# Performance work log

Hardware: AMD Instinct MI355X
Metric: run time of the kernel (lower is better)

Reference implementation:

```python
import jax, jax.numpy as jnp
import numpy as np

B, L, D = 16, 1024, 512
MAX_LEN = 1024  # module hardcodes self.max_len = 1024


def setup_inputs() -> dict:
    key = jax.random.key(0)
    k0, k1, k2, k3, k4 = jax.random.split(key, 5)
    s = 1.0 / np.sqrt(D)
    return {
        "x": jax.random.normal(k0, (B, L, D), jnp.float32),
        "generator": 0.02 * jax.random.normal(k1, (D, 2 * MAX_LEN - 1), jnp.float32),
        "Wq": jax.random.normal(k2, (D, D), jnp.float32) * s,
        "Wv": jax.random.normal(k3, (D, D), jnp.float32) * s,
        "Wc": jax.random.normal(k4, (D, D), jnp.float32) * s,
    }


def reference(x, generator, Wq, Wv, Wc):
    Bc, Lc, Dc = x.shape
    q = x @ Wq.T                      # (B, L, D)
    v = x @ Wv.T                      # (B, L, D)
    # extract_center_window: window of size 2L-1 centered at MAX_LEN-1
    center_full = (generator.shape[-1] + 1) // 2  # == MAX_LEN
    gen = generator[:, center_full - Lc: center_full + Lc - 1]  # (D, 2L-1)
    w = jnp.einsum('bld,di->bli', q, gen)  # (B, L, 2L-1)
    # Toeplitz gather: out[b, l, i] = w[b, l, (L-1) - l + i]
    r = jnp.arange(Lc)
    idx = (Lc - 1) - r[:, None] + r[None, :]  # (L, L)
    w = jnp.take_along_axis(w, idx[None, :, :], axis=-1)  # (B, L, L)
    w = jnp.cumsum(w, axis=1)
    w = jax.nn.relu(w)
    w = jnp.tril(w)
    w = w / (jnp.sum(w, axis=-1, keepdims=True) + 1e-8)
    out = jnp.einsum('bli,bid->bld', w, v)  # (B, L, D)
    return out @ Wc.T
```

## Files before the change

kernel.cpp:

```cpp
#include <hip/hip_runtime.h>
#include <hip/hip_bf16.h>

typedef __attribute__((ext_vector_type(8))) __bf16 bf16x8;
typedef __attribute__((ext_vector_type(4))) __bf16 bf16x4;
typedef __attribute__((ext_vector_type(4))) float  f32x4;

__device__ __forceinline__ void gl_lds16(const __bf16* g, __bf16* l) {
  __builtin_amdgcn_global_load_lds(
      (const __attribute__((address_space(1))) void*)g,
      (__attribute__((address_space(3))) void*)l,
      16, 0, 0);
}


__global__ __launch_bounds__(256) void prep_kernel(
    const float* __restrict__ x, const float* __restrict__ gen,
    const float* __restrict__ Wq, const float* __restrict__ Wv, const float* __restrict__ Wc,
    __bf16* __restrict__ xb, __bf16* __restrict__ genT,
    __bf16* __restrict__ wqT, __bf16* __restrict__ wvT, __bf16* __restrict__ wcb,
    float* __restrict__ gp) {
  __shared__ float S[64][65];
  const int blk = blockIdx.x, tid = threadIdx.x;

  if (blk < 128) {
    const float* in = (blk < 64) ? Wq : Wv;
    __bf16* out = (blk < 64) ? wqT : wvT;
    int t = blk & 63;
    int tx = tid & 63, ty = tid >> 6;
    int d0 = (t >> 3) * 64, e0 = (t & 7) * 64;
#pragma unroll
    for (int i = 0; i < 16; ++i) {
      int di = i * 4 + ty;
      S[di][tx] = in[(long)(d0 + di) * 512 + e0 + tx];
    }
    __syncthreads();
#pragma unroll
    for (int i = 0; i < 16; ++i) {
      int ei = i * 4 + ty;
      out[(long)(e0 + ei) * 512 + d0 + tx] = (__bf16)S[tx][ei];
    }
  } else if (blk < 384) {
    int i = (blk - 128) * 256 + tid;
    float4 v = ((const float4*)Wc)[i];
    bf16x4 o;
    o[0] = (__bf16)v.x; o[1] = (__bf16)v.y; o[2] = (__bf16)v.z; o[3] = (__bf16)v.w;
    *(bf16x4*)(wcb + 4L * i) = o;
  } else if (blk < 2432) {
    int i = blk - 384;
    for (int d = tid; d < 512; d += 256) {
      float v = (i < 2047) ? gen[(long)d * 2047 + i] : 0.f;
      genT[(long)i * 512 + d] = (__bf16)v;
    }
  } else if (blk < 10624) {
    int i = (blk - 2432) * 256 + tid;
    float4 v = ((const float4*)x)[i];
    bf16x4 o;
    o[0] = (__bf16)v.x; o[1] = (__bf16)v.y; o[2] = (__bf16)v.z; o[3] = (__bf16)v.w;
    *(bf16x4*)(xb + 4L * i) = o;
  } else {
    int t = blk - 10624;
    int i = t % 63, c = t / 63;
    int d0 = c * 64, k = tid;
    float a0 = 0.f, a1 = 0.f;
#pragma unroll 8
    for (int u = 0; u < 64; ++u) {
      int d = d0 + u;
      float g = gen[(long)d * 2047 + 992 + i];
      a0 += Wq[(long)d * 512 + k] * g;
      a1 += Wq[(long)d * 512 + k + 256] * g;
    }
    long o = ((long)c * 63 + i) * 512;
    gp[o + k] = a0;
    gp[o + k + 256] = a1;
  }
}

__global__ void g2t_reduce(const float* __restrict__ gp, float* __restrict__ g2t) {
  int idx = blockIdx.x * 256 + threadIdx.x;
  if (idx >= 63 * 512) return;
  float s = 0.f;
#pragma unroll
  for (int c = 0; c < 8; ++c) s += gp[(long)c * 63 * 512 + idx];
  g2t[idx] = s;
}

__device__ __forceinline__ void gemm128_body(
    const __bf16* __restrict__ Ab, const __bf16* __restrict__ Bb,
    __bf16 (*As)[128 * 32], __bf16 (*Bs)[128 * 32],
    int m0, int n0, int K, int nt, f32x4 (&acc)[4][4]) {
  const int tid = threadIdx.x;
  const int w = tid >> 6, l = tid & 63;
  const int srow = w * 16 + (l >> 2);
  const int scol = (((l & 3) ^ ((l >> 3) & 3))) * 8;
  const int wr = (w >> 1) * 64, wc = (w & 1) * 64;
  const int fr = l & 15;
  const int cp = (((l >> 4) ^ ((fr >> 1) & 3))) << 3;

  auto STAGE = [&](int t, int p) {
    const int k0 = t << 5;
    gl_lds16(Ab + (long)(m0 + srow) * K + (k0 + scol),      &As[p][(w * 16) * 32]);
    gl_lds16(Ab + (long)(m0 + 64 + srow) * K + (k0 + scol), &As[p][(64 + w * 16) * 32]);
    gl_lds16(Bb + (long)(n0 + srow) * K + (k0 + scol),      &Bs[p][(w * 16) * 32]);
    gl_lds16(Bb + (long)(n0 + 64 + srow) * K + (k0 + scol), &Bs[p][(64 + w * 16) * 32]);
  };
  STAGE(0, 0);
  if (nt > 1) STAGE(1, 1);
  if (nt > 2) STAGE(2, 2);
  int p = 0;
  for (int t = 0; t < nt; ++t) {
    const int ahead = nt - 1 - t;
    if (ahead >= 2)      asm volatile("s_waitcnt vmcnt(8)\ns_barrier" ::: "memory");
    else if (ahead == 1) asm volatile("s_waitcnt vmcnt(4)\ns_barrier" ::: "memory");
    else                 asm volatile("s_waitcnt vmcnt(0)\ns_barrier" ::: "memory");
    bf16x8 af[4], bg[4];
#pragma unroll
    for (int i = 0; i < 4; ++i) af[i] = *(const bf16x8*)&As[p][(wr + i * 16 + fr) * 32 + cp];
#pragma unroll
    for (int j = 0; j < 4; ++j) bg[j] = *(const bf16x8*)&Bs[p][(wc + j * 16 + fr) * 32 + cp];
    asm volatile("s_waitcnt lgkmcnt(0)\ns_barrier" ::: "memory");
    if (t + 3 < nt) STAGE(t + 3, p);
#pragma unroll
    for (int i = 0; i < 4; ++i)
#pragma unroll
      for (int j = 0; j < 4; ++j)
        acc[i][j] = __builtin_amdgcn_mfma_f32_16x16x32_bf16(af[i], bg[j], acc[i][j], 0, 0, 0);
    p = (p == 2) ? 0 : p + 1;
  }
}

__global__ __launch_bounds__(256) void gemm_fold(
    const __bf16* __restrict__ A1, const __bf16* __restrict__ B1, __bf16* __restrict__ C1,
    const __bf16* __restrict__ A2, const __bf16* __restrict__ B2, __bf16* __restrict__ C2) {
  __shared__ __bf16 As[3][128 * 32];
  __shared__ __bf16 Bs[3][128 * 32];
  const int b = blockIdx.x;
  const __bf16 *Ab, *Bb; __bf16* C; int m0, n0;
  if (b < 16) { Ab = A1; Bb = B1; C = C1; m0 = (b >> 2) * 128; n0 = (b & 3) * 128; }
  else { int t = b - 16; Ab = A2; Bb = B2; C = C2; m0 = (t >> 2) * 128; n0 = (t & 3) * 128; }

  f32x4 acc[4][4] = {};
  gemm128_body(Ab, Bb, As, Bs, m0, n0, 512, 16, acc);

  const int l = threadIdx.x & 63, w = threadIdx.x >> 6;
  const int rbase = m0 + (w >> 1) * 64 + ((l >> 4) << 2);
  const int cbase = n0 + (w & 1) * 64 + (l & 15);
#pragma unroll
  for (int i = 0; i < 4; ++i)
#pragma unroll
    for (int r = 0; r < 4; ++r) {
      long row = rbase + i * 16 + r;
#pragma unroll
      for (int j = 0; j < 4; ++j) C[row * 512 + cbase + j * 16] = (__bf16)acc[i][j][r];
    }
}

__global__ __launch_bounds__(256) void gemm_out(
    const __bf16* __restrict__ A, const __bf16* __restrict__ B, float* __restrict__ Cv,
    const float* __restrict__ aux) {
  __shared__ __bf16 As[3][128 * 32];
  __shared__ __bf16 Bs[3][128 * 32];
  const int m0 = blockIdx.y * 128, n0 = blockIdx.x * 128, bz = blockIdx.z;
  const int K = 1024;
  const __bf16* Ab = A + (long)bz * 1024 * 1024;
  const __bf16* Bb = B + (long)bz * 512 * 1024;
  const int nt = (m0 + 128) >> 5;

  f32x4 acc[4][4] = {};
  gemm128_body(Ab, Bb, As, Bs, m0, n0, K, nt, acc);

  const int l = threadIdx.x & 63, w = threadIdx.x >> 6;
  const int rbase = m0 + (w >> 1) * 64 + ((l >> 4) << 2);
  const int cbase = n0 + (w & 1) * 64 + (l & 15);
  float* C = Cv + (long)bz * 512 * 1024;
  const float* ax = aux + bz * 1024;
#pragma unroll
  for (int i = 0; i < 4; ++i)
#pragma unroll
    for (int r = 0; r < 4; ++r) {
      long row = rbase + i * 16 + r;
      float sc = 1.f / (ax[row] + 1e-8f);
#pragma unroll
      for (int j = 0; j < 4; ++j) C[row * 512 + cbase + j * 16] = acc[i][j][r] * sc;
    }
}

__global__ __launch_bounds__(512) void gemm_x(
    const __bf16* __restrict__ A, const __bf16* __restrict__ Bg,
    const __bf16* __restrict__ Pm, __bf16* __restrict__ S, __bf16* __restrict__ vT) {
  __shared__ __bf16 As[3][256 * 32];
  __shared__ __bf16 Bs[3][128 * 32];
  const int tid = threadIdx.x;
  const int w = tid >> 6, l = tid & 63;

  int wgid = blockIdx.x;
  int swz = (wgid & 7) * 112 + (wgid >> 3);
  int y = swz / 14, xt = swz - y * 14;
  const bool band = (xt < 10);
  const int m0 = y * 256;
  const int n0 = band ? (6 - 2 * (y & 3) + xt) * 128 : (xt - 10) * 128;
  const __bf16* Bb = band ? Bg : Pm;
  const int K = 512;

  const int srow = w * 16 + (l >> 2);
  const int scol = (((l & 3) ^ ((l >> 3) & 3))) * 8;
  const int wr = (w >> 1) * 64;
  const int wc = (w & 1) * 64;
  const int fr = l & 15;
  const int cp = (((l >> 4) ^ ((fr >> 1) & 3))) << 3;

  f32x4 acc[4][4] = {};

  auto STAGE = [&](int t, int p) {
    const int k0 = t << 5;
    gl_lds16(A + (long)(m0 + srow) * K + (k0 + scol),        &As[p][(w * 16) * 32]);
    gl_lds16(A + (long)(m0 + 128 + srow) * K + (k0 + scol),  &As[p][(128 + w * 16) * 32]);
    gl_lds16(Bb + (long)(n0 + srow) * K + (k0 + scol),       &Bs[p][(w * 16) * 32]);
  };

  STAGE(0, 0);
  STAGE(1, 1);
  STAGE(2, 2);

  int p = 0;
  for (int t = 0; t < 16; ++t) {
    const int ahead = 15 - t;
    if (ahead >= 2)      asm volatile("s_waitcnt vmcnt(6)\ns_barrier" ::: "memory");
    else if (ahead == 1) asm volatile("s_waitcnt vmcnt(3)\ns_barrier" ::: "memory");
    else                 asm volatile("s_waitcnt vmcnt(0)\ns_barrier" ::: "memory");
    bf16x8 af[4], bg[4];
#pragma unroll
    for (int i = 0; i < 4; ++i) af[i] = *(const bf16x8*)&As[p][(wr + i * 16 + fr) * 32 + cp];
#pragma unroll
    for (int j = 0; j < 4; ++j) bg[j] = *(const bf16x8*)&Bs[p][(wc + j * 16 + fr) * 32 + cp];
    asm volatile("s_waitcnt lgkmcnt(0)\ns_barrier" ::: "memory");
    if (t + 3 < 16) STAGE(t + 3, p);
#pragma unroll
    for (int i = 0; i < 4; ++i)
#pragma unroll
      for (int j = 0; j < 4; ++j)
        acc[i][j] = __builtin_amdgcn_mfma_f32_16x16x32_bf16(af[i], bg[j], acc[i][j], 0, 0, 0);
    p = (p == 2) ? 0 : p + 1;
  }

  const int rbase = m0 + wr + ((l >> 4) << 2);
  const int cbase = n0 + wc + fr;

  if (band) {
#pragma unroll
    for (int i = 0; i < 4; ++i)
#pragma unroll
      for (int r = 0; r < 4; ++r) {
        int row = rbase + i * 16 + r;
        int lloc = row & 1023;
#pragma unroll
        for (int j = 0; j < 4; ++j) {
          int jj = cbase + j * 16 - 1023 + lloc;
          if ((unsigned)jj < 1024u)
            S[(long)row * 1024 + jj] = (__bf16)acc[i][j][r];
        }
      }
  } else {
#pragma unroll
    for (int i = 0; i < 4; ++i) {
      int gm = rbase + i * 16;
      int bt = gm >> 10, lloc = gm & 1023;
#pragma unroll
      for (int j = 0; j < 4; ++j) {
        bf16x4 pk;
        pk[0] = (__bf16)acc[i][j][0]; pk[1] = (__bf16)acc[i][j][1];
        pk[2] = (__bf16)acc[i][j][2]; pk[3] = (__bf16)acc[i][j][3];
        *(bf16x4*)&vT[((long)bt * 512 + cbase + j * 16) * 1024 + lloc] = pk;
      }
    }
  }
}

__global__ __launch_bounds__(128) void chunk_sums(const __bf16* __restrict__ S,
                                                  float* __restrict__ csum,
                                                  float* __restrict__ rowsum) {
  int j0 = threadIdx.x * 8;
  int c = blockIdx.x, b = blockIdx.y;
  if (c < 8) rowsum[b * 1024 + c * 128 + threadIdx.x] = 0.f;
  const __bf16* Sb = S + (long)b * 1024 * 1024;
  float a[8] = {};
  int l0 = c * 16;
  for (int l = l0; l < l0 + 16; ++l) {
    bf16x8 v = *(const bf16x8*)&Sb[(long)l * 1024 + j0];
#pragma unroll
    for (int k = 0; k < 8; ++k) a[k] += (float)v[k];
  }
  long o = ((long)(b * 64 + c) << 10) + j0;
#pragma unroll
  for (int k = 0; k < 8; ++k) csum[o + k] = a[k];
}

__global__ __launch_bounds__(256) void scan_dots(
    float* __restrict__ csum,
    const float* __restrict__ x, const float* __restrict__ g2t, float* __restrict__ Sg) {
  const int blk = blockIdx.x, tid = threadIdx.x;
  if (blk < 64) {
    int idx = blk * 256 + tid;
    int b = idx >> 10, j = idx & 1023;
    long base = ((long)b * 64 << 10) + j;
    float v[64];
#pragma unroll
    for (int c = 0; c < 64; ++c) v[c] = csum[base + ((long)c << 10)];
    float s = 0.f;
#pragma unroll
    for (int c = 0; c < 64; ++c) { csum[base + ((long)c << 10)] = s; s += v[c]; }
  } else {
    int gid = (blk - 64) * 4 + (tid >> 6);
    int lane = tid & 63;
    int b = gid >> 10, rem = gid & 1023, m = rem >> 5, j = rem & 31;
    const float4* xr = (const float4*)(x + ((long)b * 1024 + m) * 512);
    const float4* gr = (const float4*)(g2t + (long)(31 - m + j) * 512);
    float4 a0 = xr[lane * 2], a1 = xr[lane * 2 + 1];
    float4 c0 = gr[lane * 2], c1 = gr[lane * 2 + 1];
    float s = a0.x * c0.x + a0.y * c0.y + a0.z * c0.z + a0.w * c0.w
            + a1.x * c1.x + a1.y * c1.y + a1.z * c1.z + a1.w * c1.w;
#pragma unroll
    for (int off = 32; off; off >>= 1) s += __shfl_down(s, off);
    if (lane == 0) Sg[gid] = s;
  }
}

__global__ __launch_bounds__(128) void cumsum_relu(const __bf16* __restrict__ S,
                                                   const float* __restrict__ csum,
                                                   __bf16* __restrict__ wrelu,
                                                   float* __restrict__ rowsum) {
  int j0 = threadIdx.x * 8;
  int c = blockIdx.x, b = blockIdx.y;
  float run[8];
  long co = ((long)(b * 64 + c) << 10) + j0;
#pragma unroll
  for (int k = 0; k < 8; ++k) run[k] = csum[co + k];
  const __bf16* Sb = S + (long)b * 1024 * 1024;
  __bf16* wr = wrelu + (long)b * 1024 * 1024;
  int l0 = c * 16;
  for (int l = l0; l < l0 + 16; ++l) {
    bf16x8 v = *(const bf16x8*)&Sb[(long)l * 1024 + j0];
    bf16x8 o;
    float rs = 0.f;
#pragma unroll
    for (int k = 0; k < 8; ++k) {
      run[k] += (float)v[k];
      float val = (j0 + k <= l) ? fmaxf(run[k], 0.f) : 0.f;
      o[k] = (__bf16)val;
      rs += val;
    }
    if (j0 < (((l >> 7) + 1) << 7))
      *(bf16x8*)&wr[(long)l * 1024 + j0] = o;
#pragma unroll
    for (int off = 32; off; off >>= 1) rs += __shfl_down(rs, off);
    if ((threadIdx.x & 63) == 0 && rs != 0.f) atomicAdd(&rowsum[b * 1024 + l], rs);
  }
}

__global__ __launch_bounds__(1024) void small_scan(
    const float* __restrict__ Sg, __bf16* __restrict__ wrelu, float* __restrict__ rowsum) {
  int b = blockIdx.x, tid = threadIdx.x;
  __shared__ float S[32][33];
  int m = tid >> 5, j = tid & 31;
  S[m][j] = Sg[b * 1024 + tid];
  __syncthreads();
  if (tid < 32) {
    float run = 0.f;
    for (int mm = 0; mm < 32; ++mm) { run += S[mm][tid]; S[mm][tid] = run; }
  }
  __syncthreads();
  float v = (j <= m) ? fmaxf(S[m][j], 0.f) : 0.f;
  wrelu[((long)b * 1024 + m) * 1024 + j] = (__bf16)v;
  float rs = v;
#pragma unroll
  for (int off = 16; off; off >>= 1) rs += __shfl_down(rs, off, 32);
  if (j == 0) rowsum[b * 1024 + m] = rs;
}

extern "C" void kernel_launch(void* const* d_in, const int* in_sizes, int n_in,
                              void* d_out, int out_size, void* d_ws, size_t ws_size,
                              hipStream_t stream) {
  const float* x   = (const float*)d_in[0];
  const float* gen = (const float*)d_in[1];
  const float* Wq  = (const float*)d_in[2];
  const float* Wv  = (const float*)d_in[3];
  const float* Wc  = (const float*)d_in[4];

  char* ws = (char*)d_ws;
  __bf16* xb    = (__bf16*)(ws + 0L);
  __bf16* vT    = (__bf16*)(ws + 33554432L);
  __bf16* Smat  = (__bf16*)(ws + 67108864L);
  __bf16* wrelu = (__bf16*)(ws + 134217728L);
  __bf16* genT  = (__bf16*)(ws + 167772160L);
  __bf16* wqT   = (__bf16*)(ws + 169869312L);
  __bf16* wvT   = (__bf16*)(ws + 170393600L);
  __bf16* wcb   = (__bf16*)(ws + 170917888L);
  float*  g2t   = (float*)(ws + 171442176L);
  float*  csum  = (float*)(ws + 16777216L);
  float*  rsum  = (float*)(ws + 16777216L + 4194304L);
  float*  Sbuf  = (float*)(ws + 16777216L + 4259840L);
  __bf16* Pmat  = (__bf16*)(ws + 50331648L);
  __bf16* Bg    = (__bf16*)(ws + 51380224L);
  float*  gp    = (float*)(ws + 58720256L);

  prep_kernel<<<11128, 256, 0, stream>>>(x, gen, Wq, Wv, Wc, xb, genT, wqT, wvT, wcb, gp);
  g2t_reduce<<<126, 256, 0, stream>>>(gp, g2t);

  gemm_fold<<<80, 256, 0, stream>>>(wcb, wvT, Pmat, genT, wqT, Bg);

  gemm_x<<<896, 512, 0, stream>>>(xb, Bg, Pmat, Smat, vT);

  chunk_sums<<<dim3(64, 16), 128, 0, stream>>>(Smat, csum, rsum);
  scan_dots<<<4160, 256, 0, stream>>>(csum, x, g2t, Sbuf);
  cumsum_relu<<<dim3(64, 16), 128, 0, stream>>>(Smat, csum, wrelu, rsum);

  small_scan<<<16, 1024, 0, stream>>>(Sbuf, wrelu, rsum);

  gemm_out<<<dim3(4, 8, 16), 256, 0, stream>>>(wrelu, vT, (float*)d_out, rsum);
}
```

Baseline: 139.2 us.

## Split-K the fold GEMMs, merge reductions, absorb small_scan into cumsum_relu

The fold GEMMs (80 blocks, K=512) become split-K with 4 K-slices writing fp32 partials, followed by a separate reduction kernel that casts to bf16. The g2t reduction is folded into the same launch as extra blocks, and the small_scan kernel is removed by having cumsum_relu handle the exact small block region directly from Sbuf. gemm_out uses a 1D grid with a swizzled block order for cache locality. These changes aim to cut launch count and fill the GPU better on the small GEMM. In exchange they add fp32 partial traffic and a serial prefix loop in a few cumsum blocks.

```diff
diff --git a/kernel.cpp b/kernel.cpp
--- a/kernel.cpp
+++ b/kernel.cpp
@@ -75,15 +75,6 @@
   }
 }
 
-__global__ void g2t_reduce(const float* __restrict__ gp, float* __restrict__ g2t) {
-  int idx = blockIdx.x * 256 + threadIdx.x;
-  if (idx >= 63 * 512) return;
-  float s = 0.f;
-#pragma unroll
-  for (int c = 0; c < 8; ++c) s += gp[(long)c * 63 * 512 + idx];
-  g2t[idx] = s;
-}
-
 __device__ __forceinline__ void gemm128_body(
     const __bf16* __restrict__ Ab, const __bf16* __restrict__ Bb,
     __bf16 (*As)[128 * 32], __bf16 (*Bs)[128 * 32],
@@ -128,18 +119,35 @@
   }
 }
 
-__global__ __launch_bounds__(256) void gemm_fold(
-    const __bf16* __restrict__ A1, const __bf16* __restrict__ B1, __bf16* __restrict__ C1,
-    const __bf16* __restrict__ A2, const __bf16* __restrict__ B2, __bf16* __restrict__ C2) {
+__global__ __launch_bounds__(256) void fold_part(
+    const __bf16* __restrict__ wcb, const __bf16* __restrict__ wvT,
+    const __bf16* __restrict__ genT, const __bf16* __restrict__ wqT,
+    float* __restrict__ gpP, float* __restrict__ gpB,
+    const float* __restrict__ gp, float* __restrict__ g2t) {
+  const int blk = blockIdx.x;
+  if (blk >= 320) {
+    int idx = (blk - 320) * 256 + threadIdx.x;
+    if (idx >= 63 * 512) return;
+    float s = 0.f;
+#pragma unroll
+    for (int c = 0; c < 8; ++c) s += gp[(long)c * 63 * 512 + idx];
+    g2t[idx] = s;
+    return;
+  }
   __shared__ __bf16 As[3][128 * 32];
   __shared__ __bf16 Bs[3][128 * 32];
-  const int b = blockIdx.x;
-  const __bf16 *Ab, *Bb; __bf16* C; int m0, n0;
-  if (b < 16) { Ab = A1; Bb = B1; C = C1; m0 = (b >> 2) * 128; n0 = (b & 3) * 128; }
-  else { int t = b - 16; Ab = A2; Bb = B2; C = C2; m0 = (t >> 2) * 128; n0 = (t & 3) * 128; }
-
+  const __bf16 *Ab, *Bb; float* Cp; int m0, n0, kz;
+  if (blk < 64) {
+    int t = blk; kz = t & 3; int tl = t >> 2;
+    m0 = (tl >> 2) * 128; n0 = (tl & 3) * 128;
+    Ab = wcb; Bb = wvT; Cp = gpP + (long)kz * 262144;
+  } else {
+    int t = blk - 64; kz = t & 3; int tl = t >> 2;
+    m0 = (tl >> 2) * 128; n0 = (tl & 3) * 128;
+    Ab = genT; Bb = wqT; Cp = gpB + (long)kz * 1048576;
+  }
   f32x4 acc[4][4] = {};
-  gemm128_body(Ab, Bb, As, Bs, m0, n0, 512, 16, acc);
+  gemm128_body(Ab + kz * 128, Bb + kz * 128, As, Bs, m0, n0, 512, 4, acc);
 
   const int l = threadIdx.x & 63, w = threadIdx.x >> 6;
   const int rbase = m0 + (w >> 1) * 64 + ((l >> 4) << 2);
@@ -150,8 +158,26 @@
     for (int r = 0; r < 4; ++r) {
       long row = rbase + i * 16 + r;
 #pragma unroll
-      for (int j = 0; j < 4; ++j) C[row * 512 + cbase + j * 16] = (__bf16)acc[i][j][r];
-    }
+      for (int j = 0; j < 4; ++j) Cp[row * 512 + cbase + j * 16] = acc[i][j][r];
+    }
+}
+
+__global__ __launch_bounds__(256) void fold_red(
+    const float* __restrict__ gpP, const float* __restrict__ gpB,
+    __bf16* __restrict__ Pmat, __bf16* __restrict__ Bg) {
+  long e = ((long)blockIdx.x * 256 + threadIdx.x) * 4;
+  const float* src; __bf16* dst; long off, stride;
+  if (e < 262144) { src = gpP; dst = Pmat; off = e; stride = 262144; }
+  else { src = gpB; dst = Bg; off = e - 262144; stride = 1048576; }
+  float4 s = {0.f, 0.f, 0.f, 0.f};
+#pragma unroll
+  for (int kz = 0; kz < 4; ++kz) {
+    float4 v = *(const float4*)&src[kz * stride + off];
+    s.x += v.x; s.y += v.y; s.z += v.z; s.w += v.w;
+  }
+  bf16x4 o;
+  o[0] = (__bf16)s.x; o[1] = (__bf16)s.y; o[2] = (__bf16)s.z; o[3] = (__bf16)s.w;
+  *(bf16x4*)&dst[off] = o;
 }
 
 __global__ __launch_bounds__(256) void gemm_out(
@@ -159,7 +185,11 @@
     const float* __restrict__ aux) {
   __shared__ __bf16 As[3][128 * 32];
   __shared__ __bf16 Bs[3][128 * 32];
-  const int m0 = blockIdx.y * 128, n0 = blockIdx.x * 128, bz = blockIdx.z;
+  int bid = blockIdx.x;
+  int swz = (bid & 7) * 64 + (bid >> 3);
+  int xn = swz & 3, tt = swz >> 2;
+  int yn = tt & 7, bz = tt >> 3;
+  const int m0 = yn * 128, n0 = xn * 128;
   const int K = 1024;
   const __bf16* Ab = A + (long)bz * 1024 * 1024;
   const __bf16* Bb = B + (long)bz * 512 * 1024;
@@ -326,27 +356,47 @@
 
 __global__ __launch_bounds__(128) void cumsum_relu(const __bf16* __restrict__ S,
                                                    const float* __restrict__ csum,
+                                                   const float* __restrict__ Sx,
                                                    __bf16* __restrict__ wrelu,
                                                    float* __restrict__ rowsum) {
   int j0 = threadIdx.x * 8;
   int c = blockIdx.x, b = blockIdx.y;
+  const bool exact = (c < 2) && (j0 < 32);
   float run[8];
-  long co = ((long)(b * 64 + c) << 10) + j0;
-#pragma unroll
-  for (int k = 0; k < 8; ++k) run[k] = csum[co + k];
+  if (exact) {
+#pragma unroll
+    for (int k = 0; k < 8; ++k) run[k] = 0.f;
+    for (int m = 0; m < c * 16; ++m)
+#pragma unroll
+      for (int k = 0; k < 8; ++k) run[k] += Sx[b * 1024 + m * 32 + j0 + k];
+  } else {
+    long co = ((long)(b * 64 + c) << 10) + j0;
+#pragma unroll
+    for (int k = 0; k < 8; ++k) run[k] = csum[co + k];
+  }
   const __bf16* Sb = S + (long)b * 1024 * 1024;
   __bf16* wr = wrelu + (long)b * 1024 * 1024;
   int l0 = c * 16;
   for (int l = l0; l < l0 + 16; ++l) {
-    bf16x8 v = *(const bf16x8*)&Sb[(long)l * 1024 + j0];
     bf16x8 o;
     float rs = 0.f;
-#pragma unroll
-    for (int k = 0; k < 8; ++k) {
-      run[k] += (float)v[k];
-      float val = (j0 + k <= l) ? fmaxf(run[k], 0.f) : 0.f;
-      o[k] = (__bf16)val;
-      rs += val;
+    if (exact) {
+#pragma unroll
+      for (int k = 0; k < 8; ++k) {
+        run[k] += Sx[b * 1024 + l * 32 + j0 + k];
+        float val = (j0 + k <= l) ? fmaxf(run[k], 0.f) : 0.f;
+        o[k] = (__bf16)val;
+        rs += val;
+      }
+    } else {
+      bf16x8 v = *(const bf16x8*)&Sb[(long)l * 1024 + j0];
+#pragma unroll
+      for (int k = 0; k < 8; ++k) {
+        run[k] += (float)v[k];
+        float val = (j0 + k <= l) ? fmaxf(run[k], 0.f) : 0.f;
+        o[k] = (__bf16)val;
+        rs += val;
+      }
     }
     if (j0 < (((l >> 7) + 1) << 7))
       *(bf16x8*)&wr[(long)l * 1024 + j0] = o;
@@ -354,26 +404,6 @@
     for (int off = 32; off; off >>= 1) rs += __shfl_down(rs, off);
     if ((threadIdx.x & 63) == 0 && rs != 0.f) atomicAdd(&rowsum[b * 1024 + l], rs);
   }
-}
-
-__global__ __launch_bounds__(1024) void small_scan(
-    const float* __restrict__ Sg, __bf16* __restrict__ wrelu, float* __restrict__ rowsum) {
-  int b = blockIdx.x, tid = threadIdx.x;
-  __shared__ float S[32][33];
-  int m = tid >> 5, j = tid & 31;
-  S[m][j] = Sg[b * 1024 + tid];
-  __syncthreads();
-  if (tid < 32) {
-    float run = 0.f;
-    for (int mm = 0; mm < 32; ++mm) { run += S[mm][tid]; S[mm][tid] = run; }
-  }
-  __syncthreads();
-  float v = (j <= m) ? fmaxf(S[m][j], 0.f) : 0.f;
-  wrelu[((long)b * 1024 + m) * 1024 + j] = (__bf16)v;
-  float rs = v;
-#pragma unroll
-  for (int off = 16; off; off >>= 1) rs += __shfl_down(rs, off, 32);
-  if (j == 0) rowsum[b * 1024 + m] = rs;
 }
 
 extern "C" void kernel_launch(void* const* d_in, const int* in_sizes, int n_in,
@@ -401,19 +431,19 @@
   __bf16* Pmat  = (__bf16*)(ws + 50331648L);
   __bf16* Bg    = (__bf16*)(ws + 51380224L);
   float*  gp    = (float*)(ws + 58720256L);
+  float*  gpP   = (float*)(ws + 134217728L);
+  float*  gpB   = (float*)(ws + 134217728L + 4194304L);
 
   prep_kernel<<<11128, 256, 0, stream>>>(x, gen, Wq, Wv, Wc, xb, genT, wqT, wvT, wcb, gp);
-  g2t_reduce<<<126, 256, 0, stream>>>(gp, g2t);
-
-  gemm_fold<<<80, 256, 0, stream>>>(wcb, wvT, Pmat, genT, wqT, Bg);
+
+  fold_part<<<446, 256, 0, stream>>>(wcb, wvT, genT, wqT, gpP, gpB, gp, g2t);
+  fold_red<<<1280, 256, 0, stream>>>(gpP, gpB, Pmat, Bg);
 
   gemm_x<<<896, 512, 0, stream>>>(xb, Bg, Pmat, Smat, vT);
 
   chunk_sums<<<dim3(64, 16), 128, 0, stream>>>(Smat, csum, rsum);
   scan_dots<<<4160, 256, 0, stream>>>(csum, x, g2t, Sbuf);
-  cumsum_relu<<<dim3(64, 16), 128, 0, stream>>>(Smat, csum, wrelu, rsum);
-
-  small_scan<<<16, 1024, 0, stream>>>(Sbuf, wrelu, rsum);
-
-  gemm_out<<<dim3(4, 8, 16), 256, 0, stream>>>(wrelu, vT, (float*)d_out, rsum);
-}
+  cumsum_relu<<<dim3(64, 16), 128, 0, stream>>>(Smat, csum, Sbuf, wrelu, rsum);
+
+  gemm_out<<<512, 256, 0, stream>>>(wrelu, vT, (float*)d_out, rsum);
+}
```

Result: no change. 141.3 us (+1.5%).
